# Kernel optimization log

Hardware: AMD Instinct MI355X
Metric: run time of the kernel (lower is better)

The kernel has to match this reference:

```python
import jax, jax.numpy as jnp
import numpy as np

H = 64  # hidden size

def _lstm_forward(x, W_ih, W_hh, b_ih, b_hh):
    # x: [B, T, 1]; PyTorch gate order: i, f, g, o
    B = x.shape[0]
    # precompute input contribution for all timesteps: [B, T, 4H]
    x_gates = jnp.einsum('bti,gi->btg', x, W_ih) + b_ih + b_hh

    def step(carry, xg):
        h, c = carry                      # [B, H] each
        gates = xg + h @ W_hh.T           # [B, 4H]
        i = jax.nn.sigmoid(gates[:, 0*H:1*H])
        f = jax.nn.sigmoid(gates[:, 1*H:2*H])
        g = jnp.tanh(gates[:, 2*H:3*H])
        o = jax.nn.sigmoid(gates[:, 3*H:4*H])
        c_new = f * c + i * g
        h_new = o * jnp.tanh(c_new)
        return (h_new, c_new), None

    h0 = jnp.zeros((B, H), dtype=x.dtype)
    c0 = jnp.zeros((B, H), dtype=x.dtype)
    (h_last, _), _ = jax.lax.scan(step, (h0, c0), jnp.swapaxes(x_gates, 0, 1))
    return h_last

def setup_inputs() -> dict:
    key = jax.random.key(0)
    ks = jax.random.split(key, 7)
    B, T = 262144, 5
    s = 1.0 / np.sqrt(H)  # pytorch LSTM default init scale
    return {
        'x':    jax.random.normal(ks[0], (B, T, 1), dtype=jnp.float32),
        'W_ih': jax.random.uniform(ks[1], (4*H, 1), jnp.float32, -s, s),
        'W_hh': jax.random.uniform(ks[2], (4*H, H), jnp.float32, -s, s),
        'b_ih': jax.random.uniform(ks[3], (4*H,), jnp.float32, -s, s),
        'b_hh': jax.random.uniform(ks[4], (4*H,), jnp.float32, -s, s),
        'W_fc': jax.random.uniform(ks[5], (1, H), jnp.float32, -s, s),
        'b_fc': jax.random.uniform(ks[6], (1,), jnp.float32, -s, s),
    }

def reference(x, W_ih, W_hh, b_ih, b_hh, W_fc, b_fc):
    h_last = _lstm_forward(x, W_ih, W_hh, b_ih, b_hh)  # [B, H]
    return h_last @ W_fc.T + b_fc                      # [B, 1]
```

## Files before the change

kernel.cpp:

```cpp
#include <hip/hip_runtime.h>

#define HDIM   64
#define TSTEPS 5
#define WAVES  8
#define BLOCK  (WAVES * 64)
#define EPW    16
#define EPB    (WAVES * EPW)

typedef _Float16 f16x8 __attribute__((ext_vector_type(8)));
typedef float    f32x4 __attribute__((ext_vector_type(4)));

#define L2E 1.44269504088896340736f

__device__ __forceinline__ float rcp_(float x) { return __builtin_amdgcn_rcpf(x); }
__device__ __forceinline__ float ex2_(float x) { return __builtin_amdgcn_exp2f(x); }
__device__ __forceinline__ float sigp_(float v) { return rcp_(1.0f + ex2_(-v)); }

__global__ __launch_bounds__(BLOCK, 3) void lstm_mfma_kernel(
    const float* __restrict__ x,
    const float* __restrict__ W_ih,
    const float* __restrict__ W_hh,
    const float* __restrict__ b_ih,
    const float* __restrict__ b_hh,
    const float* __restrict__ W_fc,
    const float* __restrict__ b_fc,
    float* __restrict__ out,
    int B)
{
    __shared__ _Float16 Wf[2048 * 8];
    __shared__ _Float16 hbuf[WAVES * 1024];
    __shared__ float    wih_s[256];
    __shared__ float    cb_s[256];
    __shared__ float    wfc_s[64];

    const int tid = threadIdx.x;

    #pragma unroll
    for (int s0 = 0; s0 < 2048; s0 += BLOCK) {
        const int s  = s0 + tid;
        const int ln = s & 63;
        const int kh = (s >> 6) & 1;
        const int n  = s >> 7;
        const float scl = ((n >> 2) == 2) ? (2.0f * L2E) : L2E;
        const int j  = n * 16 + (ln & 15);
        const int k0 = kh * 32 + ((ln >> 4) & 3) * 8;
        const float* src = W_hh + j * HDIM + k0;
        #pragma unroll
        for (int i = 0; i < 8; i++)
            Wf[s * 8 + i] = (_Float16)(src[i] * scl);
    }
    if (tid < 256) {
        const float scl = ((tid >> 6) == 2) ? (2.0f * L2E) : L2E;
        wih_s[tid] = W_ih[tid] * scl;
        cb_s[tid]  = (b_ih[tid] + b_hh[tid]) * scl;
    }
    if (tid < 64) wfc_s[tid] = W_fc[tid];
    __syncthreads();

    const int lane = tid & 63;
    const int wave = tid >> 6;
    const int m    = lane & 15;
    const int q    = lane >> 4;
    const int eg0  = (blockIdx.x * WAVES + wave) * EPW;

    _Float16* hb = hbuf + wave * 1024;

    const float* xp[4];
    #pragma unroll
    for (int r = 0; r < 4; r++) {
        int e = eg0 + q * 4 + r;
        if (e >= B) e = B - 1;
        xp[r] = x + (long)e * TSTEPS;
    }

    float c[16];
    float pfc[4];

    #pragma unroll
    for (int t = 0; t < TSTEPS; t++) {
        float xt[4];
        #pragma unroll
        for (int r = 0; r < 4; r++) xt[r] = xp[r][t];

        f16x8 hA0, hA1;
        if (t > 0) {
            hA0 = *(const f16x8*)(hb + lane * 8);
            hA1 = *(const f16x8*)(hb + 512 + lane * 8);
        }

        #pragma unroll
        for (int gr = 0; gr < 4; gr++) {
            float wihv[4], cbv[4];
            #pragma unroll
            for (int G = 0; G < 4; G++) {
                wihv[G] = wih_s[G * 64 + gr * 16 + m];
                cbv[G]  = cb_s[G * 64 + gr * 16 + m];
            }
            f32x4 ag[4];
            #pragma unroll
            for (int G = 0; G < 4; G++)
                #pragma unroll
                for (int r = 0; r < 4; r++)
                    ag[G][r] = fmaf(xt[r], wihv[G], cbv[G]);

            if (t > 0) {
                #pragma unroll
                for (int G = 0; G < 4; G++) {
                    const int n = G * 4 + gr;
                    f16x8 w0 = *(const f16x8*)(Wf + (n * 2 + 0) * 512 + lane * 8);
                    f16x8 w1 = *(const f16x8*)(Wf + (n * 2 + 1) * 512 + lane * 8);
                    ag[G] = __builtin_amdgcn_mfma_f32_16x16x32_f16(hA0, w0, ag[G], 0, 0, 0);
                    ag[G] = __builtin_amdgcn_mfma_f32_16x16x32_f16(hA1, w1, ag[G], 0, 0, 0);
                }
            }

            #pragma unroll
            for (int r = 0; r < 4; r++) {
                const int u = gr * 4 + r;
                const float Ei = ex2_(-ag[0][r]);
                const float Eg = ex2_(ag[2][r]);
                const float it = (2.0f * L2E) * (Eg - 1.0f) *
                                 rcp_((1.0f + Ei) * (Eg + 1.0f));
                float cs = it;
                if (t > 0) {
                    const float sf = sigp_(ag[1][r]);
                    cs = fmaf(sf, c[u], it);
                }
                c[u] = cs;
                const float Eo = ex2_(-ag[3][r]);
                const float Ec = ex2_(cs);
                const float hn = (Ec - 1.0f) * rcp_((1.0f + Eo) * (Ec + 1.0f));
                if (t < TSTEPS - 1) {
                    const int lp = (q * 4 + r) + 16 * (2 * (gr & 1) + (m >> 3));
                    hb[(gr >> 1) * 512 + lp * 8 + (m & 7)] = (_Float16)hn;
                } else {
                    const float w = wfc_s[gr * 16 + m];
                    pfc[r] = (gr == 0) ? hn * w : fmaf(hn, w, pfc[r]);
                }
            }
            __builtin_amdgcn_sched_barrier(0);
        }
    }

    const float bfc = b_fc[0];
    #pragma unroll
    for (int r = 0; r < 4; r++) {
        float p = pfc[r];
        p += __shfl_xor(p, 1, 64);
        p += __shfl_xor(p, 2, 64);
        p += __shfl_xor(p, 4, 64);
        p += __shfl_xor(p, 8, 64);
        if (m == 0) {
            const int e = eg0 + q * 4 + r;
            if (e < B) out[e] = p + bfc;
        }
    }
}

extern "C" void kernel_launch(void* const* d_in, const int* in_sizes, int n_in,
                              void* d_out, int out_size, void* d_ws, size_t ws_size,
                              hipStream_t stream) {
    const float* x    = (const float*)d_in[0];
    const float* W_ih = (const float*)d_in[1];
    const float* W_hh = (const float*)d_in[2];
    const float* b_ih = (const float*)d_in[3];
    const float* b_hh = (const float*)d_in[4];
    const float* W_fc = (const float*)d_in[5];
    const float* b_fc = (const float*)d_in[6];
    float* out = (float*)d_out;

    const int B = in_sizes[0] / TSTEPS;
    const int grid = (B + EPB - 1) / EPB;
    lstm_mfma_kernel<<<grid, BLOCK, 0, stream>>>(x, W_ih, W_hh, b_ih, b_hh,
                                                 W_fc, b_fc, out, B);
}
```

Baseline: 152.7 us.

## Raise occupancy, merge sigmoid reciprocals, drop sched barrier, share x pointer

Raises the launch-bounds occupancy hint from 3 to 4 blocks per CU. It computes the input and forget gate values from one shared reciprocal instead of two, cutting transcendental ops. It also removes the per-group scheduling barrier so the compiler can interleave MFMA and math across groups, and replaces four per-row x pointers with one base pointer. The higher occupancy target may force register spills. The clamped base pointer also shifts rows in a partial last tile, which changes which outputs are written when B is not a multiple of 4.

After: 151.8 us, median of 2. No clear change (-0.6%).

```diff
diff --git a/kernel.cpp b/kernel.cpp
--- a/kernel.cpp
+++ b/kernel.cpp
@@ -14,9 +14,8 @@
 
 __device__ __forceinline__ float rcp_(float x) { return __builtin_amdgcn_rcpf(x); }
 __device__ __forceinline__ float ex2_(float x) { return __builtin_amdgcn_exp2f(x); }
-__device__ __forceinline__ float sigp_(float v) { return rcp_(1.0f + ex2_(-v)); }
 
-__global__ __launch_bounds__(BLOCK, 3) void lstm_mfma_kernel(
+__global__ __launch_bounds__(BLOCK, 4) void lstm_mfma_kernel(
     const float* __restrict__ x,
     const float* __restrict__ W_ih,
     const float* __restrict__ W_hh,
@@ -65,13 +64,9 @@
 
     _Float16* hb = hbuf + wave * 1024;
 
-    const float* xp[4];
-    #pragma unroll
-    for (int r = 0; r < 4; r++) {
-        int e = eg0 + q * 4 + r;
-        if (e >= B) e = B - 1;
-        xp[r] = x + (long)e * TSTEPS;
-    }
+    int e0 = eg0 + q * 4;
+    if (e0 > B - 4) e0 = (B >= 4 ? B - 4 : 0);
+    const float* xp0 = x + (long)e0 * TSTEPS;
 
     float c[16];
     float pfc[4];
@@ -80,7 +75,7 @@
     for (int t = 0; t < TSTEPS; t++) {
         float xt[4];
         #pragma unroll
-        for (int r = 0; r < 4; r++) xt[r] = xp[r][t];
+        for (int r = 0; r < 4; r++) xt[r] = xp0[r * TSTEPS + t];
 
         f16x8 hA0, hA1;
         if (t > 0) {
@@ -119,12 +114,18 @@
                 const int u = gr * 4 + r;
                 const float Ei = ex2_(-ag[0][r]);
                 const float Eg = ex2_(ag[2][r]);
-                const float it = (2.0f * L2E) * (Eg - 1.0f) *
-                                 rcp_((1.0f + Ei) * (Eg + 1.0f));
-                float cs = it;
+                const float a  = (1.0f + Ei) * (Eg + 1.0f);
+                const float gn = (2.0f * L2E) * (Eg - 1.0f);
+                float cs;
                 if (t > 0) {
-                    const float sf = sigp_(ag[1][r]);
+                    const float Ef = ex2_(-ag[1][r]);
+                    const float b  = 1.0f + Ef;
+                    const float rr = rcp_(a * b);
+                    const float it = gn * (rr * b);
+                    const float sf = rr * a;
                     cs = fmaf(sf, c[u], it);
+                } else {
+                    cs = gn * rcp_(a);
                 }
                 c[u] = cs;
                 const float Eo = ex2_(-ag[3][r]);
@@ -138,7 +139,6 @@
                     pfc[r] = (gr == 0) ? hn * w : fmaf(hn, w, pfc[r]);
                 }
             }
-            __builtin_amdgcn_sched_barrier(0);
         }
     }
 
@@ -151,7 +151,7 @@
         p += __shfl_xor(p, 4, 64);
         p += __shfl_xor(p, 8, 64);
         if (m == 0) {
-            const int e = eg0 + q * 4 + r;
+            const int e = e0 + r;
             if (e < B) out[e] = p + bfc;
         }
     }
```
